# Kernel tuning notes

Hardware: AMD Instinct MI355X
Metric: run time of the kernel (lower is better)

Reference implementation:

```python
import jax, jax.numpy as jnp
import numpy as np

B, S, HID = 2, 2048, 2048
NH, HD = 16, 128            # num heads, head dim (HID = NH*HD)
ROT = 64                    # rotary_dim
MASK_VALUE = -10000.0


def _rotate_every_two(x):
    # x: [..., d] with d even; interleaved (-x2, x1)
    x1 = x[..., ::2]
    x2 = x[..., 1::2]
    return jnp.stack((-x2, x1), axis=-1).reshape(x.shape)


def _fixed_sincos(seq_len, dim):
    inv_freq = 1.0 / (10000.0 ** (jnp.arange(0, dim, 2, dtype=jnp.float32) / dim))
    t = jnp.arange(seq_len, dtype=jnp.float32)
    ang = t[:, None] * inv_freq[None, :]          # [S, dim/2]
    return jnp.sin(ang), jnp.cos(ang)


def _apply_rope(x, sin, cos):
    # x: [B, S, H, rot]; sin/cos: [S, rot/2] -> repeat_interleave(2) -> [S, rot]
    sin = jnp.repeat(sin, 2, axis=-1)[None, :, None, :]
    cos = jnp.repeat(cos, 2, axis=-1)[None, :, None, :]
    return x * cos + _rotate_every_two(x) * sin


def setup_inputs() -> dict:
    key = jax.random.key(0)
    ks = jax.random.split(key, 7)
    w_scale = 1.0 / np.sqrt(HID)
    return {
        "hidden_states": jax.random.normal(ks[0], (B, S, HID), dtype=jnp.float32),
        "attention_mask": jnp.zeros((B, 1, 1, S), dtype=jnp.float32),
        "Wq": jax.random.normal(ks[1], (HID, HID), dtype=jnp.float32) * w_scale,
        "bq": jnp.zeros((HID,), dtype=jnp.float32),
        "Wk": jax.random.normal(ks[2], (HID, HID), dtype=jnp.float32) * w_scale,
        "bk": jnp.zeros((HID,), dtype=jnp.float32),
        "Wv": jax.random.normal(ks[3], (HID, HID), dtype=jnp.float32) * w_scale,
        "bv": jnp.zeros((HID,), dtype=jnp.float32),
    }


def reference(hidden_states, attention_mask, Wq, bq, Wk, bk, Wv, bv):
    # QKV projections (torch Linear: x @ W.T + b)
    q = (hidden_states @ Wq.T + bq).reshape(B, S, NH, HD)
    k = (hidden_states @ Wk.T + bk).reshape(B, S, NH, HD)
    v = (hidden_states @ Wv.T + bv).reshape(B, S, NH, HD)

    # Inline rotary on first ROT dims of q/k
    sin, cos = _fixed_sincos(S, ROT)
    q = jnp.concatenate([_apply_rope(q[..., :ROT], sin, cos), q[..., ROT:]], axis=-1)
    k = jnp.concatenate([_apply_rope(k[..., :ROT], sin, cos), k[..., ROT:]], axis=-1)

    # Scores [B, H, S, S]
    scores = jnp.einsum('bqhd,bkhd->bhqk', q, k) / np.sqrt(HD)

    # Causal mask + additive attention mask
    causal = jnp.tril(jnp.ones((S, S), dtype=bool))[None, None]
    scores = jnp.where(causal, scores, jnp.asarray(MASK_VALUE, scores.dtype))
    scores = scores + attention_mask

    probs = jax.nn.softmax(scores, axis=-1)
    ctx = jnp.einsum('bhqk,bkhd->bqhd', probs, v)
    return ctx.reshape(B, S, HID)
```

## Files before the change

kernel.cpp:

```cpp
#include <hip/hip_runtime.h>

typedef unsigned short bhalf;
typedef __attribute__((ext_vector_type(4))) float    f32x4;
typedef __attribute__((ext_vector_type(8))) short    s16x8;
typedef __attribute__((ext_vector_type(4))) float    floatx4;
typedef __attribute__((ext_vector_type(4))) unsigned short u16x4;

#define B_  2
#define S_  2048
#define HID_ 2048
#define NH_ 16
#define HD_ 128
#define M_  (B_*S_)
#define MASKV (-10000.0f)

__device__ __forceinline__ bhalf f32_to_bf16(float f) {
    union { float f; unsigned int u; } v; v.f = f;
    unsigned int r = v.u + 0x7FFFu + ((v.u >> 16) & 1u);
    return (bhalf)(r >> 16);
}
__device__ __forceinline__ bhalf f32_to_bf16_trunc(float f) {
    union { float f; unsigned int u; } v; v.f = f;
    return (bhalf)(v.u >> 16);
}
__device__ __forceinline__ float bf16_to_f32(bhalf h) {
    union { unsigned int u; float f; } v; v.u = ((unsigned int)h) << 16;
    return v.f;
}

__device__ __forceinline__ void gl_lds16(const void* g, void* l) {
    __builtin_amdgcn_global_load_lds(
        (const __attribute__((address_space(1))) void*)g,
        (__attribute__((address_space(3))) void*)l, 16, 0, 0);
}

#define BARRIER() asm volatile("s_barrier" ::: "memory")

__global__ __launch_bounds__(256) void cast_all(const float* __restrict__ hs,
                                                const float* __restrict__ Wq,
                                                const float* __restrict__ Wk,
                                                const float* __restrict__ Wv,
                                                bhalf* __restrict__ dst) {
    int idx = blockIdx.x * 256 + threadIdx.x;
    const float* src;
    if (idx < 2097152)      src = hs + (size_t)idx * 4;
    else if (idx < 3145728) src = Wq + (size_t)(idx - 2097152) * 4;
    else if (idx < 4194304) src = Wk + (size_t)(idx - 3145728) * 4;
    else                    src = Wv + (size_t)(idx - 4194304) * 4;
    floatx4 f = *(const floatx4*)src;
    u16x4 o;
    o.x = f32_to_bf16(f.x); o.y = f32_to_bf16(f.y);
    o.z = f32_to_bf16(f.z); o.w = f32_to_bf16(f.w);
    *(u16x4*)(dst + (size_t)idx * 4) = o;
}

__global__ __launch_bounds__(512, 2) void qkv_gemm(const bhalf* __restrict__ A,
                                                   const bhalf* __restrict__ Wb,
                                                   const float* __restrict__ bq,
                                                   const float* __restrict__ bk,
                                                   const float* __restrict__ bv,
                                                   bhalf* __restrict__ Out,
                                                   bhalf* __restrict__ VTo) {
    __shared__ __align__(16) bhalf As[2][16384];
    __shared__ __align__(16) bhalf Bs[2][16384];
    const int tid  = threadIdx.x;
    const int lane = tid & 63, w = tid >> 6;
    const int quad = lane >> 4, l = lane & 15;
    const int wy = w >> 2, wx = w & 3;
    const int m0 = blockIdx.x * 256, n0 = blockIdx.y * 256;
    const int z  = blockIdx.z;
    const bhalf* W    = Wb + (size_t)z * HID_ * HID_;
    const float* bias = (z == 0) ? bq : (z == 1) ? bk : bv;
    bhalf* out        = Out + (size_t)z * M_ * HID_;

    bhalf* AsF = &As[0][0];
    bhalf* BsF = &Bs[0][0];

    const int row_s = tid >> 3;
    const int kg_s  = (tid & 7) ^ (row_s & 7);
    const int w512  = w * 512;

    const bhalf* gA0 = A + (size_t)(m0 +   0 + row_s) * HID_ + kg_s * 8;
    const bhalf* gA1 = A + (size_t)(m0 +  64 + row_s) * HID_ + kg_s * 8;
    const bhalf* gA2 = A + (size_t)(m0 + 128 + row_s) * HID_ + kg_s * 8;
    const bhalf* gA3 = A + (size_t)(m0 + 192 + row_s) * HID_ + kg_s * 8;
    const bhalf* gB0 = W + (size_t)(n0 +   0 + row_s) * HID_ + kg_s * 8;
    const bhalf* gB1 = W + (size_t)(n0 +  64 + row_s) * HID_ + kg_s * 8;
    const bhalf* gB2 = W + (size_t)(n0 + 128 + row_s) * HID_ + kg_s * 8;
    const bhalf* gB3 = W + (size_t)(n0 + 192 + row_s) * HID_ + kg_s * 8;

    const int aIdx = (wy * 128 + l) * 64;
    const int bIdx = (wx * 64  + l) * 64;
    const int swz0 = ((0 + quad) ^ (l & 7)) * 8;
    const int swz1 = ((4 + quad) ^ (l & 7)) * 8;

    f32x4 acc[8][4] = {};

#define ADV() do { gA0 += 64; gA1 += 64; gA2 += 64; gA3 += 64;               \
                   gB0 += 64; gB1 += 64; gB2 += 64; gB3 += 64; } while (0)

#define KTILE(BUF, ST1, ST2, VM) do {                                        \
    const int CB = (BUF) * 16384, NB = ((BUF) ^ 1) * 16384;                  \
    s16x8 a_[4][2], b01_[2][2], b23_[2][2];                                  \
                    \
    _Pragma("unroll") for (int mt = 0; mt < 4; ++mt) {                       \
        a_[mt][0] = *(const s16x8*)(AsF + CB + aIdx + mt * 1024 + swz0);     \
        a_[mt][1] = *(const s16x8*)(AsF + CB + aIdx + mt * 1024 + swz1); }   \
    _Pragma("unroll") for (int nt = 0; nt < 2; ++nt) {                       \
        b01_[nt][0] = *(const s16x8*)(BsF + CB + bIdx + nt * 1024 + swz0);   \
        b01_[nt][1] = *(const s16x8*)(BsF + CB + bIdx + nt * 1024 + swz1); } \
    if (ST1) { gl_lds16(gA1 + 64, AsF + NB + 1 * 4096 + w512);               \
               gl_lds16(gA3 + 64, AsF + NB + 3 * 4096 + w512); }             \
    BARRIER();                                                               \
    __builtin_amdgcn_s_setprio(1);                                           \
    _Pragma("unroll") for (int mt = 0; mt < 4; ++mt)                         \
      _Pragma("unroll") for (int nt = 0; nt < 2; ++nt)                       \
        _Pragma("unroll") for (int ks = 0; ks < 2; ++ks)                     \
          acc[mt][nt] = __builtin_amdgcn_mfma_f32_16x16x32_bf16(             \
              a_[mt][ks], b01_[nt][ks], acc[mt][nt], 0, 0, 0);               \
    __builtin_amdgcn_s_setprio(0);                                           \
    BARRIER();                                                               \
                           \
    _Pragma("unroll") for (int nt = 0; nt < 2; ++nt) {                       \
        b23_[nt][0] = *(const s16x8*)(BsF + CB + bIdx + (nt+2)*1024 + swz0); \
        b23_[nt][1] = *(const s16x8*)(BsF + CB + bIdx + (nt+2)*1024 + swz1);}\
    if (ST2) { gl_lds16(gA0 + 128, AsF + CB + 0 * 4096 + w512);              \
               gl_lds16(gA2 + 128, AsF + CB + 2 * 4096 + w512); }            \
    BARRIER();                                                               \
    __builtin_amdgcn_s_setprio(1);                                           \
    _Pragma("unroll") for (int mt = 0; mt < 4; ++mt)                         \
      _Pragma("unroll") for (int nt = 0; nt < 2; ++nt)                       \
        _Pragma("unroll") for (int ks = 0; ks < 2; ++ks)                     \
          acc[mt][nt + 2] = __builtin_amdgcn_mfma_f32_16x16x32_bf16(         \
              a_[mt][ks], b23_[nt][ks], acc[mt][nt + 2], 0, 0, 0);           \
    __builtin_amdgcn_s_setprio(0);                                           \
    BARRIER();                                                               \
                        \
    _Pragma("unroll") for (int mt = 0; mt < 4; ++mt) {                       \
        a_[mt][0] = *(const s16x8*)(AsF + CB + aIdx + 4096 + mt*1024 + swz0);\
        a_[mt][1] = *(const s16x8*)(AsF + CB + aIdx + 4096 + mt*1024 + swz1);}\
    if (ST2) { gl_lds16(gB0 + 128, BsF + CB + 0 * 4096 + w512);              \
               gl_lds16(gB1 + 128, BsF + CB + 1 * 4096 + w512); }            \
    BARRIER();                                                               \
    __builtin_amdgcn_s_setprio(1);                                           \
    _Pragma("unroll") for (int mt = 0; mt < 4; ++mt)                         \
      _Pragma("unroll") for (int nt = 0; nt < 2; ++nt)                       \
        _Pragma("unroll") for (int ks = 0; ks < 2; ++ks)                     \
          acc[4 + mt][nt + 2] = __builtin_amdgcn_mfma_f32_16x16x32_bf16(     \
              a_[mt][ks], b23_[nt][ks], acc[4 + mt][nt + 2], 0, 0, 0);       \
    __builtin_amdgcn_s_setprio(0);                                           \
    BARRIER();                                                               \
    \
    if (ST2) { gl_lds16(gB2 + 128, BsF + CB + 2 * 4096 + w512);              \
               gl_lds16(gB3 + 128, BsF + CB + 3 * 4096 + w512); }            \
    if ((VM) == 6)      asm volatile("s_waitcnt vmcnt(6)" ::: "memory");     \
    else if ((VM) == 0) asm volatile("s_waitcnt vmcnt(0)" ::: "memory");     \
    BARRIER();                                                               \
    __builtin_amdgcn_s_setprio(1);                                           \
    _Pragma("unroll") for (int mt = 0; mt < 4; ++mt)                         \
      _Pragma("unroll") for (int nt = 0; nt < 2; ++nt)                       \
        _Pragma("unroll") for (int ks = 0; ks < 2; ++ks)                     \
          acc[4 + mt][nt] = __builtin_amdgcn_mfma_f32_16x16x32_bf16(         \
              a_[mt][ks], b01_[nt][ks], acc[4 + mt][nt], 0, 0, 0);           \
    __builtin_amdgcn_s_setprio(0);                                           \
    BARRIER();                                                               \
} while (0)

    gl_lds16(gA0, AsF + 0 * 4096 + w512);
    gl_lds16(gA2, AsF + 2 * 4096 + w512);
    gl_lds16(gB0, BsF + 0 * 4096 + w512);
    gl_lds16(gB1, BsF + 1 * 4096 + w512);
    gl_lds16(gB2, BsF + 2 * 4096 + w512);
    gl_lds16(gB3, BsF + 3 * 4096 + w512);
    gl_lds16(gA1, AsF + 1 * 4096 + w512);
    gl_lds16(gA3, AsF + 3 * 4096 + w512);
    gl_lds16(gA0 + 64, AsF + 16384 + 0 * 4096 + w512);
    gl_lds16(gA2 + 64, AsF + 16384 + 2 * 4096 + w512);
    gl_lds16(gB0 + 64, BsF + 16384 + 0 * 4096 + w512);
    gl_lds16(gB1 + 64, BsF + 16384 + 1 * 4096 + w512);
    gl_lds16(gB2 + 64, BsF + 16384 + 2 * 4096 + w512);
    gl_lds16(gB3 + 64, BsF + 16384 + 3 * 4096 + w512);
    asm volatile("s_waitcnt vmcnt(6)" ::: "memory");
    BARRIER();

    for (int tt = 0; tt < 15; ++tt) {
        KTILE(0, 1, 1, 6); ADV();
        KTILE(1, 1, 1, 6); ADV();
    }
    KTILE(0, 1, 0, 0); ADV();
    KTILE(1, 0, 0, -1);

#undef KTILE
#undef ADV

    if (z == 2) {
#pragma unroll
        for (int mt = 0; mt < 8; ++mt) {
#pragma unroll
            for (int nt = 0; nt < 4; ++nt) {
                int col = n0 + wx * 64 + nt * 16 + l;
                float bv_ = bias[col];
                int row0 = m0 + wy * 128 + mt * 16 + quad * 4;
                int bb = row0 >> 11, s0 = row0 & 2047;
                u16x4 o;
#pragma unroll
                for (int r = 0; r < 4; ++r) o[r] = f32_to_bf16(acc[mt][nt][r] + bv_);
                *(u16x4*)(VTo + ((size_t)(bb * 16) * 128 + col) * S_ + s0) = o;
            }
        }
    } else {
#pragma unroll
        for (int mt = 0; mt < 8; ++mt) {
#pragma unroll
            for (int nt = 0; nt < 4; ++nt) {
                int col = n0 + wx * 64 + nt * 16 + l;
                float bv_ = bias[col];
#pragma unroll
                for (int r = 0; r < 4; ++r) {
                    int row = m0 + wy * 128 + mt * 16 + quad * 4 + r;
                    out[(size_t)row * HID_ + col] = f32_to_bf16(acc[mt][nt][r] + bv_);
                }
            }
        }
    }
}

__global__ __launch_bounds__(256) void rope_table(float2* __restrict__ tab) {
    int idx = blockIdx.x * 256 + threadIdx.x;
    int i = idx & 31, s = idx >> 5;
    float inv = expf(-(float)i * 0.2878231366242557f);
    float ang = (float)s * inv;
    tab[idx] = make_float2(sinf(ang), cosf(ang));
}

__global__ __launch_bounds__(256) void rope_apply(bhalf* __restrict__ Qb,
                                                  bhalf* __restrict__ Kb,
                                                  const float2* __restrict__ tab) {
    int flat = blockIdx.x * 256 + threadIdx.x;
    int i = flat & 31;
    int h = (flat >> 5) & 15;
    int s = (flat >> 9) & 2047;
    int b = flat >> 20;
    size_t base = ((size_t)(b * S_ + s)) * HID_ + h * HD_ + 2 * i;
    float2 sc = tab[s * 32 + i];
    float c = sc.y, sn = sc.x;
    {
        unsigned int q = *(const unsigned int*)(Qb + base);
        float x0 = bf16_to_f32((bhalf)(q & 0xffff));
        float x1 = bf16_to_f32((bhalf)(q >> 16));
        unsigned int o = (unsigned int)f32_to_bf16(x0 * c - x1 * sn)
                       | ((unsigned int)f32_to_bf16(x1 * c + x0 * sn) << 16);
        *(unsigned int*)(Qb + base) = o;
    }
    {
        unsigned int k = *(const unsigned int*)(Kb + base);
        float x0 = bf16_to_f32((bhalf)(k & 0xffff));
        float x1 = bf16_to_f32((bhalf)(k >> 16));
        unsigned int o = (unsigned int)f32_to_bf16(x0 * c - x1 * sn)
                       | ((unsigned int)f32_to_bf16(x1 * c + x0 * sn) << 16);
        *(unsigned int*)(Kb + base) = o;
    }
}

__global__ __launch_bounds__(512, 2) void flash_attn(const bhalf* __restrict__ Qb,
                                                     const bhalf* __restrict__ Kb,
                                                     const bhalf* __restrict__ VT,
                                                     const float* __restrict__ amask,
                                                     float* __restrict__ out) {
    __shared__ __align__(16) bhalf Kbuf[2][2048 * 8];
    __shared__ __align__(16) bhalf Vbuf[2][2048 * 8];
    const int tid = threadIdx.x, lane = tid & 63, w = tid >> 6;
    const int quad = lane >> 4, l = lane & 15;
    const int pr = blockIdx.x, bh = blockIdx.y;
    const int b = bh >> 4, h = bh & 15;
    s16x8 ones;
#pragma unroll
    for (int j = 0; j < 8; ++j) ones[j] = (short)0x3F80;
    const int fpl = ((l >> 2) << 1) | (l & 1);

    for (int pass = 0; pass < 2; ++pass) {
        const int jt = pass ? (15 - pr) : pr;
        const int myrow = jt * 128 + w * 16;
        const int nch = jt + 1;

        s16x8 qf[4];
        {
            const bhalf* Qrow = Qb + (size_t)(b * S_ + myrow + l) * HID_ + h * HD_;
#pragma unroll
            for (int ks = 0; ks < 4; ++ks)
                qf[ks] = *(const s16x8*)(Qrow + ks * 32 + quad * 8);
        }

        float m_run[4] = {-1e30f, -1e30f, -1e30f, -1e30f};
        f32x4 l_acc = {};
        f32x4 acc[8] = {};

        __syncthreads();

#pragma unroll
        for (int j = 0; j < 4; ++j) {
            int slot0 = j * 512 + w * 64;
            int slot  = slot0 + lane;
            int row = slot >> 4, x = slot & 15;
            int g   = (x & 8) | ((x ^ row) & 7);
            gl_lds16(Kb + (size_t)(b * S_ + row) * HID_ + h * HD_ + g * 8,
                     &Kbuf[0][slot0 * 8]);
            gl_lds16(VT + ((size_t)bh * HD_ + row) * S_ + g * 8,
                     &Vbuf[0][slot0 * 8]);
        }

        for (int kc = 0; kc < nch; ++kc) {
            const int cur = kc & 1, nxt = cur ^ 1;
            const int key0 = kc * 128;
            __syncthreads();

            const bool diag = (kc == jt);

            float am[8];
#pragma unroll
            for (int nt = 0; nt < 8; ++nt) am[nt] = amask[b * S_ + key0 + nt * 16 + l];
            if (kc + 1 < nch) {
                const int key1 = key0 + 128;
#pragma unroll
                for (int j = 0; j < 4; ++j) {
                    int slot0 = j * 512 + w * 64;
                    int slot  = slot0 + lane;
                    int row = slot >> 4, x = slot & 15;
                    int g   = (x & 8) | ((x ^ row) & 7);
                    gl_lds16(Kb + (size_t)(b * S_ + key1 + row) * HID_ + h * HD_ + g * 8,
                             &Kbuf[nxt][slot0 * 8]);
                    gl_lds16(VT + ((size_t)bh * HD_ + row) * S_ + key1 + g * 8,
                             &Vbuf[nxt][slot0 * 8]);
                }
            }

            const bhalf* Kc = &Kbuf[cur][0];
            const bhalf* Vc = &Vbuf[cur][0];
            bhalf* Pw = &Kbuf[cur][0] + w * 2048;

            f32x4 s[8] = {};
#pragma unroll
            for (int nt = 0; nt < 8; ++nt) {
                int key = nt * 16 + l;
#pragma unroll
                for (int ks = 0; ks < 4; ++ks) {
                    int dg = ks * 4 + quad;
                    int x  = (dg & 8) | ((dg ^ key) & 7);
                    s16x8 kf = *(const s16x8*)(Kc + (key * 16 + x) * 8);
                    s[nt] = __builtin_amdgcn_mfma_f32_16x16x32_bf16(qf[ks], kf, s[nt], 0, 0, 0);
                }
            }
            __asm__ __volatile__("s_waitcnt lgkmcnt(0)\n\ts_barrier" ::: "memory");

#pragma unroll
            for (int r = 0; r < 4; ++r) {
                const int qrow = myrow + quad * 4 + r;
                float p[8];
#pragma unroll
                for (int nt = 0; nt < 8; ++nt) {
                    float v = s[nt][r] * 0.08838834764831845f;
                    if (diag) { int key = key0 + nt * 16 + l; v = (key > qrow) ? MASKV : v; }
                    p[nt] = v + am[nt];
                }
                float mx = fmaxf(fmaxf(fmaxf(p[0], p[1]), fmaxf(p[2], p[3])),
                                 fmaxf(fmaxf(p[4], p[5]), fmaxf(p[6], p[7])));
#pragma unroll
                for (int msk = 1; msk < 16; msk <<= 1) mx = fmaxf(mx, __shfl_xor(mx, msk, 64));
                float m_new = fmaxf(m_run[r], mx);
                float alpha = __expf(m_run[r] - m_new);
                m_run[r] = m_new;
                const int m  = quad * 4 + r;
                const int fm = (quad << 1) | (r & 1);
#pragma unroll
                for (int nt = 0; nt < 8; ++nt) {
                    float e = __expf(p[nt] - m_new);
                    int key = nt * 16 + l;
                    Pw[(m * 16 + ((key >> 3) ^ fm)) * 8 + (key & 7)] = f32_to_bf16_trunc(e);
                }
                l_acc[r] *= alpha;
#pragma unroll
                for (int nt = 0; nt < 8; ++nt) acc[nt][r] *= alpha;
            }
#pragma unroll
            for (int kstep = 0; kstep < 4; ++kstep) {
                int kg = kstep * 4 + quad;
                s16x8 pf = *(const s16x8*)(Pw + (l * 16 + (kg ^ fpl)) * 8);
                l_acc = __builtin_amdgcn_mfma_f32_16x16x32_bf16(pf, ones, l_acc, 0, 0, 0);
#pragma unroll
                for (int nt = 0; nt < 8; ++nt) {
                    int d = nt * 16 + l;
                    int x = (kg & 8) | ((kg ^ d) & 7);
                    s16x8 vf = *(const s16x8*)(Vc + (d * 16 + x) * 8);
                    acc[nt] = __builtin_amdgcn_mfma_f32_16x16x32_bf16(pf, vf, acc[nt], 0, 0, 0);
                }
            }
        }

        float inv[4];
#pragma unroll
        for (int r = 0; r < 4; ++r) inv[r] = 1.f / l_acc[r];
#pragma unroll
        for (int nt = 0; nt < 8; ++nt) {
            int col = h * HD_ + nt * 16 + l;
#pragma unroll
            for (int r = 0; r < 4; ++r)
                out[(size_t)(b * S_ + myrow + quad * 4 + r) * HID_ + col] = acc[nt][r] * inv[r];
        }
    }
}

extern "C" void kernel_launch(void* const* d_in, const int* in_sizes, int n_in,
                              void* d_out, int out_size, void* d_ws, size_t ws_size,
                              hipStream_t stream) {
    const float* hs    = (const float*)d_in[0];
    const float* amask = (const float*)d_in[1];
    const float* Wq    = (const float*)d_in[2];
    const float* bq    = (const float*)d_in[3];
    const float* Wk    = (const float*)d_in[4];
    const float* bk    = (const float*)d_in[5];
    const float* Wv    = (const float*)d_in[6];
    const float* bv    = (const float*)d_in[7];
    float* out = (float*)d_out;

    bhalf* hsb = (bhalf*)d_ws;
    bhalf* wqb = hsb + 8388608;
    bhalf* wkb = wqb + 4194304;
    bhalf* wvb = wkb + 4194304;
    bhalf* Qb  = wvb + 4194304;
    bhalf* Kb  = Qb + 8388608;
    bhalf* VTb = Kb + 8388608;
    float2* tab = (float2*)(VTb + 8388608);

    rope_table<<<256, 256, 0, stream>>>(tab);
    cast_all<<<20480, 256, 0, stream>>>(hs, Wq, Wk, Wv, hsb);
    qkv_gemm<<<dim3(16, 8, 3), 512, 0, stream>>>(hsb, wqb, bq, bk, bv, Qb, VTb);
    rope_apply<<<8192, 256, 0, stream>>>(Qb, Kb, tab);
    flash_attn<<<dim3(8, 32), 512, 0, stream>>>(Qb, Kb, VTb, amask, out);
}
```

Measured before the change: 342.8 us.

## Halve QKV GEMM N-tile to 128 and fold rope table into cast kernel

The QKV GEMM tile shrinks from 256x256 to 256x128, so the grid doubles from 384 to 768 blocks and fills the 256 CUs more evenly, and the LDS buffer for B is halved. The warp layout becomes 4x2 and the prefetch, MFMA and waitcnt schedule is reworked to match. The rope sin/cos table kernel is merged into the cast kernel as extra blocks, removing one launch. The smaller tile lowers arithmetic intensity and raises global traffic for the A operand.

Result: faster. 335.0 us (-2.3%).

```diff
diff --git a/kernel.cpp b/kernel.cpp
--- a/kernel.cpp
+++ b/kernel.cpp
@@ -40,7 +40,16 @@
                                                 const float* __restrict__ Wq,
                                                 const float* __restrict__ Wk,
                                                 const float* __restrict__ Wv,
-                                                bhalf* __restrict__ dst) {
+                                                bhalf* __restrict__ dst,
+                                                float2* __restrict__ tab) {
+    if (blockIdx.x >= 20480) {
+        int idx = (blockIdx.x - 20480) * 256 + threadIdx.x;
+        int i = idx & 31, s = idx >> 5;
+        float inv = expf(-(float)i * 0.2878231366242557f);
+        float ang = (float)s * inv;
+        tab[idx] = make_float2(sinf(ang), cosf(ang));
+        return;
+    }
     int idx = blockIdx.x * 256 + threadIdx.x;
     const float* src;
     if (idx < 2097152)      src = hs + (size_t)idx * 4;
@@ -62,12 +71,12 @@
                                                    bhalf* __restrict__ Out,
                                                    bhalf* __restrict__ VTo) {
     __shared__ __align__(16) bhalf As[2][16384];
-    __shared__ __align__(16) bhalf Bs[2][16384];
+    __shared__ __align__(16) bhalf Bs[2][8192];
     const int tid  = threadIdx.x;
     const int lane = tid & 63, w = tid >> 6;
     const int quad = lane >> 4, l = lane & 15;
-    const int wy = w >> 2, wx = w & 3;
-    const int m0 = blockIdx.x * 256, n0 = blockIdx.y * 256;
+    const int wy = w >> 1, wx = w & 1;
+    const int m0 = blockIdx.x * 256, n0 = blockIdx.y * 128;
     const int z  = blockIdx.z;
     const bhalf* W    = Wb + (size_t)z * HID_ * HID_;
     const float* bias = (z == 0) ? bq : (z == 1) ? bk : bv;
@@ -86,106 +95,96 @@
     const bhalf* gA3 = A + (size_t)(m0 + 192 + row_s) * HID_ + kg_s * 8;
     const bhalf* gB0 = W + (size_t)(n0 +   0 + row_s) * HID_ + kg_s * 8;
     const bhalf* gB1 = W + (size_t)(n0 +  64 + row_s) * HID_ + kg_s * 8;
-    const bhalf* gB2 = W + (size_t)(n0 + 128 + row_s) * HID_ + kg_s * 8;
-    const bhalf* gB3 = W + (size_t)(n0 + 192 + row_s) * HID_ + kg_s * 8;
-
-    const int aIdx = (wy * 128 + l) * 64;
-    const int bIdx = (wx * 64  + l) * 64;
+
+    const int aIdx = (wy * 64 + l) * 64;
+    const int bIdx = (wx * 64 + l) * 64;
     const int swz0 = ((0 + quad) ^ (l & 7)) * 8;
     const int swz1 = ((4 + quad) ^ (l & 7)) * 8;
 
-    f32x4 acc[8][4] = {};
+    f32x4 acc[4][4] = {};
 
 #define ADV() do { gA0 += 64; gA1 += 64; gA2 += 64; gA3 += 64;               \
-                   gB0 += 64; gB1 += 64; gB2 += 64; gB3 += 64; } while (0)
+                   gB0 += 64; gB1 += 64; } while (0)
 
 #define KTILE(BUF, ST1, ST2, VM) do {                                        \
-    const int CB = (BUF) * 16384, NB = ((BUF) ^ 1) * 16384;                  \
+    const int CA = (BUF) * 16384, NA = ((BUF) ^ 1) * 16384;                  \
+    const int CBB = (BUF) * 8192;                                            \
     s16x8 a_[4][2], b01_[2][2], b23_[2][2];                                  \
-                    \
+              \
     _Pragma("unroll") for (int mt = 0; mt < 4; ++mt) {                       \
-        a_[mt][0] = *(const s16x8*)(AsF + CB + aIdx + mt * 1024 + swz0);     \
-        a_[mt][1] = *(const s16x8*)(AsF + CB + aIdx + mt * 1024 + swz1); }   \
+        a_[mt][0] = *(const s16x8*)(AsF + CA + aIdx + mt * 1024 + swz0);     \
+        a_[mt][1] = *(const s16x8*)(AsF + CA + aIdx + mt * 1024 + swz1); }   \
     _Pragma("unroll") for (int nt = 0; nt < 2; ++nt) {                       \
-        b01_[nt][0] = *(const s16x8*)(BsF + CB + bIdx + nt * 1024 + swz0);   \
-        b01_[nt][1] = *(const s16x8*)(BsF + CB + bIdx + nt * 1024 + swz1); } \
-    if (ST1) { gl_lds16(gA1 + 64, AsF + NB + 1 * 4096 + w512);               \
-               gl_lds16(gA3 + 64, AsF + NB + 3 * 4096 + w512); }             \
+        b01_[nt][0] = *(const s16x8*)(BsF + CBB + bIdx + nt * 1024 + swz0);  \
+        b01_[nt][1] = *(const s16x8*)(BsF + CBB + bIdx + nt * 1024 + swz1); }\
+    if (ST1) { gl_lds16(gA2 + 64, AsF + NA + 2 * 4096 + w512);               \
+               gl_lds16(gA3 + 64, AsF + NA + 3 * 4096 + w512); }             \
     BARRIER();                                                               \
     __builtin_amdgcn_s_setprio(1);                                           \
-    _Pragma("unroll") for (int mt = 0; mt < 4; ++mt)                         \
+    _Pragma("unroll") for (int mt = 0; mt < 2; ++mt)                         \
       _Pragma("unroll") for (int nt = 0; nt < 2; ++nt)                       \
         _Pragma("unroll") for (int ks = 0; ks < 2; ++ks)                     \
           acc[mt][nt] = __builtin_amdgcn_mfma_f32_16x16x32_bf16(             \
               a_[mt][ks], b01_[nt][ks], acc[mt][nt], 0, 0, 0);               \
     __builtin_amdgcn_s_setprio(0);                                           \
     BARRIER();                                                               \
-                           \
+    \
     _Pragma("unroll") for (int nt = 0; nt < 2; ++nt) {                       \
-        b23_[nt][0] = *(const s16x8*)(BsF + CB + bIdx + (nt+2)*1024 + swz0); \
-        b23_[nt][1] = *(const s16x8*)(BsF + CB + bIdx + (nt+2)*1024 + swz1);}\
-    if (ST2) { gl_lds16(gA0 + 128, AsF + CB + 0 * 4096 + w512);              \
-               gl_lds16(gA2 + 128, AsF + CB + 2 * 4096 + w512); }            \
+        b23_[nt][0] = *(const s16x8*)(BsF + CBB + bIdx + (nt+2)*1024 + swz0);\
+        b23_[nt][1] = *(const s16x8*)(BsF + CBB + bIdx + (nt+2)*1024 + swz1);}\
+    if (ST2) { gl_lds16(gA0 + 128, AsF + CA + 0 * 4096 + w512);              \
+               gl_lds16(gA1 + 128, AsF + CA + 1 * 4096 + w512); }            \
     BARRIER();                                                               \
     __builtin_amdgcn_s_setprio(1);                                           \
-    _Pragma("unroll") for (int mt = 0; mt < 4; ++mt)                         \
+    _Pragma("unroll") for (int mt = 0; mt < 2; ++mt)                         \
       _Pragma("unroll") for (int nt = 0; nt < 2; ++nt)                       \
         _Pragma("unroll") for (int ks = 0; ks < 2; ++ks)                     \
           acc[mt][nt + 2] = __builtin_amdgcn_mfma_f32_16x16x32_bf16(         \
               a_[mt][ks], b23_[nt][ks], acc[mt][nt + 2], 0, 0, 0);           \
     __builtin_amdgcn_s_setprio(0);                                           \
     BARRIER();                                                               \
-                        \
-    _Pragma("unroll") for (int mt = 0; mt < 4; ++mt) {                       \
-        a_[mt][0] = *(const s16x8*)(AsF + CB + aIdx + 4096 + mt*1024 + swz0);\
-        a_[mt][1] = *(const s16x8*)(AsF + CB + aIdx + 4096 + mt*1024 + swz1);}\
-    if (ST2) { gl_lds16(gB0 + 128, BsF + CB + 0 * 4096 + w512);              \
-               gl_lds16(gB1 + 128, BsF + CB + 1 * 4096 + w512); }            \
+                  \
+    if (ST2) { gl_lds16(gB0 + 128, BsF + CBB + 0 * 4096 + w512);             \
+               gl_lds16(gB1 + 128, BsF + CBB + 1 * 4096 + w512); }           \
     BARRIER();                                                               \
     __builtin_amdgcn_s_setprio(1);                                           \
-    _Pragma("unroll") for (int mt = 0; mt < 4; ++mt)                         \
+    _Pragma("unroll") for (int mt = 0; mt < 2; ++mt)                         \
       _Pragma("unroll") for (int nt = 0; nt < 2; ++nt)                       \
         _Pragma("unroll") for (int ks = 0; ks < 2; ++ks)                     \
-          acc[4 + mt][nt + 2] = __builtin_amdgcn_mfma_f32_16x16x32_bf16(     \
-              a_[mt][ks], b23_[nt][ks], acc[4 + mt][nt + 2], 0, 0, 0);       \
+          acc[2 + mt][nt] = __builtin_amdgcn_mfma_f32_16x16x32_bf16(         \
+              a_[2 + mt][ks], b01_[nt][ks], acc[2 + mt][nt], 0, 0, 0);       \
     __builtin_amdgcn_s_setprio(0);                                           \
     BARRIER();                                                               \
-    \
-    if (ST2) { gl_lds16(gB2 + 128, BsF + CB + 2 * 4096 + w512);              \
-               gl_lds16(gB3 + 128, BsF + CB + 3 * 4096 + w512); }            \
-    if ((VM) == 6)      asm volatile("s_waitcnt vmcnt(6)" ::: "memory");     \
+                           \
+    if ((VM) == 4)      asm volatile("s_waitcnt vmcnt(4)" ::: "memory");     \
     else if ((VM) == 0) asm volatile("s_waitcnt vmcnt(0)" ::: "memory");     \
     BARRIER();                                                               \
     __builtin_amdgcn_s_setprio(1);                                           \
-    _Pragma("unroll") for (int mt = 0; mt < 4; ++mt)                         \
+    _Pragma("unroll") for (int mt = 0; mt < 2; ++mt)                         \
       _Pragma("unroll") for (int nt = 0; nt < 2; ++nt)                       \
         _Pragma("unroll") for (int ks = 0; ks < 2; ++ks)                     \
-          acc[4 + mt][nt] = __builtin_amdgcn_mfma_f32_16x16x32_bf16(         \
-              a_[mt][ks], b01_[nt][ks], acc[4 + mt][nt], 0, 0, 0);           \
+          acc[2 + mt][nt + 2] = __builtin_amdgcn_mfma_f32_16x16x32_bf16(     \
+              a_[2 + mt][ks], b23_[nt][ks], acc[2 + mt][nt + 2], 0, 0, 0);   \
     __builtin_amdgcn_s_setprio(0);                                           \
     BARRIER();                                                               \
 } while (0)
 
     gl_lds16(gA0, AsF + 0 * 4096 + w512);
+    gl_lds16(gA1, AsF + 1 * 4096 + w512);
     gl_lds16(gA2, AsF + 2 * 4096 + w512);
+    gl_lds16(gA3, AsF + 3 * 4096 + w512);
     gl_lds16(gB0, BsF + 0 * 4096 + w512);
     gl_lds16(gB1, BsF + 1 * 4096 + w512);
-    gl_lds16(gB2, BsF + 2 * 4096 + w512);
-    gl_lds16(gB3, BsF + 3 * 4096 + w512);
-    gl_lds16(gA1, AsF + 1 * 4096 + w512);
-    gl_lds16(gA3, AsF + 3 * 4096 + w512);
     gl_lds16(gA0 + 64, AsF + 16384 + 0 * 4096 + w512);
-    gl_lds16(gA2 + 64, AsF + 16384 + 2 * 4096 + w512);
-    gl_lds16(gB0 + 64, BsF + 16384 + 0 * 4096 + w512);
-    gl_lds16(gB1 + 64, BsF + 16384 + 1 * 4096 + w512);
-    gl_lds16(gB2 + 64, BsF + 16384 + 2 * 4096 + w512);
-    gl_lds16(gB3 + 64, BsF + 16384 + 3 * 4096 + w512);
-    asm volatile("s_waitcnt vmcnt(6)" ::: "memory");
+    gl_lds16(gA1 + 64, AsF + 16384 + 1 * 4096 + w512);
+    gl_lds16(gB0 + 64, BsF + 8192 + 0 * 4096 + w512);
+    gl_lds16(gB1 + 64, BsF + 8192 + 1 * 4096 + w512);
+    asm volatile("s_waitcnt vmcnt(4)" ::: "memory");
     BARRIER();
 
     for (int tt = 0; tt < 15; ++tt) {
-        KTILE(0, 1, 1, 6); ADV();
-        KTILE(1, 1, 1, 6); ADV();
+        KTILE(0, 1, 1, 4); ADV();
+        KTILE(1, 1, 1, 4); ADV();
     }
     KTILE(0, 1, 0, 0); ADV();
     KTILE(1, 0, 0, -1);
@@ -195,12 +194,12 @@
 
     if (z == 2) {
 #pragma unroll
-        for (int mt = 0; mt < 8; ++mt) {
+        for (int mt = 0; mt < 4; ++mt) {
 #pragma unroll
             for (int nt = 0; nt < 4; ++nt) {
                 int col = n0 + wx * 64 + nt * 16 + l;
                 float bv_ = bias[col];
-                int row0 = m0 + wy * 128 + mt * 16 + quad * 4;
+                int row0 = m0 + wy * 64 + mt * 16 + quad * 4;
                 int bb = row0 >> 11, s0 = row0 & 2047;
                 u16x4 o;
 #pragma unroll
@@ -210,27 +209,19 @@
         }
     } else {
 #pragma unroll
-        for (int mt = 0; mt < 8; ++mt) {
+        for (int mt = 0; mt < 4; ++mt) {
 #pragma unroll
             for (int nt = 0; nt < 4; ++nt) {
                 int col = n0 + wx * 64 + nt * 16 + l;
                 float bv_ = bias[col];
 #pragma unroll
                 for (int r = 0; r < 4; ++r) {
-                    int row = m0 + wy * 128 + mt * 16 + quad * 4 + r;
+                    int row = m0 + wy * 64 + mt * 16 + quad * 4 + r;
                     out[(size_t)row * HID_ + col] = f32_to_bf16(acc[mt][nt][r] + bv_);
                 }
             }
         }
     }
-}
-
-__global__ __launch_bounds__(256) void rope_table(float2* __restrict__ tab) {
-    int idx = blockIdx.x * 256 + threadIdx.x;
-    int i = idx & 31, s = idx >> 5;
-    float inv = expf(-(float)i * 0.2878231366242557f);
-    float ang = (float)s * inv;
-    tab[idx] = make_float2(sinf(ang), cosf(ang));
 }
 
 __global__ __launch_bounds__(256) void rope_apply(bhalf* __restrict__ Qb,
@@ -431,9 +422,8 @@
     bhalf* VTb = Kb + 8388608;
     float2* tab = (float2*)(VTb + 8388608);
 
-    rope_table<<<256, 256, 0, stream>>>(tab);
-    cast_all<<<20480, 256, 0, stream>>>(hs, Wq, Wk, Wv, hsb);
-    qkv_gemm<<<dim3(16, 8, 3), 512, 0, stream>>>(hsb, wqb, bq, bk, bv, Qb, VTb);
+    cast_all<<<20736, 256, 0, stream>>>(hs, Wq, Wk, Wv, hsb, tab);
+    qkv_gemm<<<dim3(16, 16, 3), 512, 0, stream>>>(hsb, wqb, bq, bk, bv, Qb, VTb);
     rope_apply<<<8192, 256, 0, stream>>>(Qb, Kb, tab);
     flash_attn<<<dim3(8, 32), 512, 0, stream>>>(Qb, Kb, VTb, amask, out);
 }
```
